# Kernel tuning notes

Hardware: AMD Instinct MI355X
Metric: run time of the kernel (lower is better)

Reference implementation:

```python
import jax, jax.numpy as jnp
import numpy as np

IN_FEATURES = 512
OUT_FEATURES = 512
GRID_MIN = -2.0
GRID_MAX = 2.0
NUM_GRIDS = 8
SPLINE_SCALE = 0.1
BATCH = 16384


def setup_inputs() -> dict:
    key = jax.random.key(0)
    kx, kw = jax.random.split(key)
    x = jax.random.normal(kx, (BATCH, IN_FEATURES), dtype=jnp.float32)
    grid = jnp.linspace(GRID_MIN, GRID_MAX, NUM_GRIDS, dtype=jnp.float32)
    spline_weight = (
        jax.random.normal(kw, (IN_FEATURES * NUM_GRIDS, OUT_FEATURES), dtype=jnp.float32)
        * SPLINE_SCALE
    )
    return {"x": x, "grid": grid, "spline_weight": spline_weight}


def reference(x, grid, spline_weight):
    # denominator h = (grid_max - grid_min) / (num_grids - 1)
    h = (GRID_MAX - GRID_MIN) / (NUM_GRIDS - 1)
    # basis: [B, in_features, num_grids]
    basis = jnp.exp(-jnp.square((x[..., None] - grid) / h))
    # flatten to [B, in_features * num_grids] and GEMM
    return basis.reshape(basis.shape[0], -1) @ spline_weight
```

## Files before the change

kernel.cpp:

```cpp
#include <hip/hip_runtime.h>
#include <hip/hip_bf16.h>

#define BATCH 16384
#define IN_F 512
#define OUT_F 512
#define NG 8
#define KTOT (IN_F * NG)

#define SH    2.1019642153762872f
#define SSTEP 1.2011224087864498f
#define BC0N  4.2039284307525745f

typedef __attribute__((ext_vector_type(8))) short short8;
typedef __attribute__((ext_vector_type(4))) float f32x4;
typedef __attribute__((ext_vector_type(2))) float f32x2;
typedef __attribute__((ext_vector_type(4))) unsigned int u32x4;
typedef __attribute__((ext_vector_type(2))) unsigned int u32x2;

__device__ __forceinline__ unsigned fbits(float f) {
    union { float f; unsigned u; } v; v.f = f; return v.u;
}
__device__ __forceinline__ unsigned pack2bf(float lo, float hi) {
    unsigned a = (fbits(lo) + 0x8000u) >> 16;
    unsigned b = (fbits(hi) + 0x8000u) & 0xFFFF0000u;
    return a | b;
}

__global__ void wt_convert(const float* __restrict__ W, unsigned short* __restrict__ Wt) {
    const int gid  = blockIdx.x * 4 + (threadIdx.x >> 6);
    const int lane = threadIdx.x & 63;
    const int kw = gid & 511;
    const int nw = gid >> 9;
    const int n  = nw * 64 + lane;
    const int k0 = kw * 8;
    float v[8];
#pragma unroll
    for (int j = 0; j < 8; ++j)
        v[j] = W[(size_t)(k0 + j) * OUT_F + n];
    u32x4 pk;
#pragma unroll
    for (int j = 0; j < 4; ++j)
        pk[j] = pack2bf(v[2 * j], v[2 * j + 1]);
    *(u32x4*)(Wt + (size_t)n * KTOT + k0) = pk;
}

#define BM2 64
#define BN2 256
#define BK2 64
#define ABUF (BM2 * BK2)
#define BBUF (BN2 * BK2)

__global__ __launch_bounds__(256, 2) void gauss_gemm3(
        const float* __restrict__ X, const unsigned short* __restrict__ Wt,
        float* __restrict__ Out) {
    __shared__ __align__(16) unsigned short sA[2 * ABUF];
    __shared__ __align__(16) unsigned short sB[2 * BBUF];

    const int tid  = threadIdx.x;
    const int lane = tid & 63;
    const int wave = tid >> 6;
    const int rb = blockIdx.x >> 1;
    const int cb = blockIdx.x & 1;
    const int m0 = rb * BM2;
    const int n0 = cb * BN2;
    const int l15 = lane & 15;
    const int lq  = lane >> 4;

    const int arow = tid >> 2;
    const int axp  = tid & 3;
    const float* xp = X + (size_t)(m0 + arow) * IN_F + 2 * axp;
    const int aoff0 = arow * BK2 + ((((axp << 1)    ) ^ (arow & 7)) << 3);
    const int aoff1 = arow * BK2 + ((((axp << 1) | 1) ^ (arow & 7)) << 3);

    const int brow = lane >> 3;
    const int bch  = (lane & 7) ^ brow;
    const unsigned short* bsrc =
        Wt + (size_t)(n0 + wave * 64 + brow) * KTOT + bch * 8;

    f32x4 acc[4][4];
#pragma unroll
    for (int i = 0; i < 4; ++i)
#pragma unroll
        for (int j = 0; j < 4; ++j)
            acc[i][j] = (f32x4){0.f, 0.f, 0.f, 0.f};

    auto stageB = [&](int kt, int buf) {
#pragma unroll
        for (int p = 0; p < 8; ++p) {
            __builtin_amdgcn_global_load_lds(
                (const __attribute__((address_space(1))) unsigned int*)
                    (const void*)(bsrc + (size_t)p * 8 * KTOT + (size_t)kt * BK2),
                (__attribute__((address_space(3))) unsigned int*)
                    (void*)(sB + buf * BBUF + (wave * 64 + p * 8) * BK2),
                16, 0, 0);
        }
    };

    auto stageA = [&](f32x2 xv, int buf) {
        unsigned short* base = sA + buf * ABUF;
#pragma unroll
        for (int h = 0; h < 2; ++h) {
            const float xs = (h ? xv.y : xv.x) * SH;
            u32x4 pk;
#pragma unroll
            for (int g = 0; g < 8; g += 2) {
                float t0 = xs + (BC0N - g * SSTEP);
                float t1 = xs + (BC0N - (g + 1) * SSTEP);
                unsigned u0 = fbits(__builtin_amdgcn_exp2f(-t0 * t0)) + 0x8000u;
                unsigned u1 = fbits(__builtin_amdgcn_exp2f(-t1 * t1)) + 0x8000u;
                pk[g >> 1] = __builtin_amdgcn_perm(u1, u0, 0x07060302u);
            }
            *(u32x4*)(base + (h ? aoff1 : aoff0)) = pk;
        }
    };

    stageB(0, 0);
    f32x2 xv = *(const f32x2*)(xp);
    stageA(xv, 0);
    f32x2 xnext = *(const f32x2*)(xp + 8);
    __syncthreads();

    for (int kt = 0; kt < KTOT / BK2 - 1; ++kt) {
        const int cur = kt & 1, nxt = cur ^ 1;

        f32x2 xpf;
        if (kt < KTOT / BK2 - 2)
            xpf = *(const f32x2*)(xp + (size_t)(kt + 2) * 8);

        stageB(kt + 1, nxt);

        short8 af[2][4], bfv[2][4];
#pragma unroll
        for (int kk = 0; kk < 2; ++kk) {
            const int koff = ((((kk << 2) + lq) ^ (l15 & 7)) << 3);
#pragma unroll
            for (int i = 0; i < 4; ++i)
                af[kk][i] = *(const short8*)(sA + cur * ABUF + (i * 16 + l15) * BK2 + koff);
#pragma unroll
            for (int j = 0; j < 4; ++j)
                bfv[kk][j] = *(const short8*)(sB + cur * BBUF + (wave * 64 + j * 16 + l15) * BK2 + koff);
        }

        stageA(xnext, nxt);

#pragma unroll
        for (int kk = 0; kk < 2; ++kk)
#pragma unroll
            for (int i = 0; i < 4; ++i)
#pragma unroll
                for (int j = 0; j < 4; ++j)
                    acc[i][j] = __builtin_amdgcn_mfma_f32_16x16x32_bf16(af[kk][i], bfv[kk][j], acc[i][j], 0, 0, 0);

        xnext = xpf;
        __syncthreads();
    }

    {
        const int cur = (KTOT / BK2 - 1) & 1;
#pragma unroll
        for (int kk = 0; kk < 2; ++kk) {
            const int koff = ((((kk << 2) + lq) ^ (l15 & 7)) << 3);
            short8 af[4], bfv[4];
#pragma unroll
            for (int i = 0; i < 4; ++i)
                af[i] = *(const short8*)(sA + cur * ABUF + (i * 16 + l15) * BK2 + koff);
#pragma unroll
            for (int j = 0; j < 4; ++j)
                bfv[j] = *(const short8*)(sB + cur * BBUF + (wave * 64 + j * 16 + l15) * BK2 + koff);
#pragma unroll
            for (int i = 0; i < 4; ++i)
#pragma unroll
                for (int j = 0; j < 4; ++j)
                    acc[i][j] = __builtin_amdgcn_mfma_f32_16x16x32_bf16(af[i], bfv[j], acc[i][j], 0, 0, 0);
        }
    }

#pragma unroll
    for (int i = 0; i < 4; ++i) {
        const int r0 = m0 + i * 16 + lq * 4;
#pragma unroll
        for (int j = 0; j < 4; ++j) {
            const int c = n0 + wave * 64 + j * 16 + l15;
#pragma unroll
            for (int e = 0; e < 4; ++e)
                Out[(size_t)(r0 + e) * OUT_F + c] = acc[i][j][e];
        }
    }
}

#define BM 128
#define BN 128
#define BK 64
#define LDA 72
#define LDB 72

__global__ __launch_bounds__(256, 2) void gauss_gemm_fb(
        const float* __restrict__ X, const float* __restrict__ W,
        float* __restrict__ Out) {
    __shared__ __align__(16) unsigned short sA[BM * LDA];
    __shared__ __align__(16) unsigned short sB[BN * LDB];

    const int tid  = threadIdx.x;
    const int lane = tid & 63;
    const int wave = tid >> 6;
    const int rb = blockIdx.x >> 2;
    const int cb = blockIdx.x & 3;
    const int m0 = rb * BM;
    const int n0 = cb * BN;
    const int wr = (wave >> 1) * 64;
    const int wc = (wave & 1) * 64;
    const int l15 = lane & 15;
    const int lq  = lane >> 4;

    f32x4 acc[4][4];
#pragma unroll
    for (int i = 0; i < 4; ++i)
#pragma unroll
        for (int j = 0; j < 4; ++j)
            acc[i][j] = (f32x4){0.f, 0.f, 0.f, 0.f};

    const int arow = tid & 127;
    const int axq  = tid >> 7;

    for (int kt = 0; kt < KTOT / BK; ++kt) {
        const int k0  = kt * BK;
        const int xc0 = kt * (BK / NG);

        const f32x4 xv = *(const f32x4*)(X + (size_t)(m0 + arow) * IN_F + xc0 + 4 * axq);
        unsigned short* sArow = sA + arow * LDA + axq * 32;
#pragma unroll
        for (int j = 0; j < 4; ++j) {
            const float xs = xv[j] * SH;
            u32x4 pk;
#pragma unroll
            for (int g = 0; g < 8; g += 2) {
                float t0 = xs + (BC0N - g * SSTEP);
                float t1 = xs + (BC0N - (g + 1) * SSTEP);
                unsigned u0 = fbits(__builtin_amdgcn_exp2f(-t0 * t0)) + 0x8000u;
                unsigned u1 = fbits(__builtin_amdgcn_exp2f(-t1 * t1)) + 0x8000u;
                pk[g >> 1] = __builtin_amdgcn_perm(u1, u0, 0x07060302u);
            }
            *(u32x4*)(sArow + j * 8) = pk;
        }

#pragma unroll
        for (int p = 0; p < 8; ++p) {
            int id = p * 256 + tid;
            int n  = id & 127;
            int k4 = id >> 7;
            const float* wp = W + (size_t)(k0 + k4 * 4) * OUT_F + n0 + n;
            u32x2 v;
            v[0] = pack2bf(wp[0], wp[OUT_F]);
            v[1] = pack2bf(wp[2 * OUT_F], wp[3 * OUT_F]);
            *(u32x2*)(sB + n * LDB + k4 * 4) = v;
        }

        __syncthreads();

#pragma unroll
        for (int kk = 0; kk < BK; kk += 32) {
            short8 af[4], bfv[4];
#pragma unroll
            for (int i = 0; i < 4; ++i)
                af[i] = *(const short8*)(sA + (wr + i * 16 + l15) * LDA + kk + lq * 8);
#pragma unroll
            for (int i = 0; i < 4; ++i)
                bfv[i] = *(const short8*)(sB + (wc + i * 16 + l15) * LDB + kk + lq * 8);
#pragma unroll
            for (int i = 0; i < 4; ++i)
#pragma unroll
                for (int j = 0; j < 4; ++j)
                    acc[i][j] = __builtin_amdgcn_mfma_f32_16x16x32_bf16(af[i], bfv[j], acc[i][j], 0, 0, 0);
        }

        __syncthreads();
    }

#pragma unroll
    for (int i = 0; i < 4; ++i) {
        const int r0 = m0 + wr + i * 16 + lq * 4;
#pragma unroll
        for (int j = 0; j < 4; ++j) {
            const int c = n0 + wc + j * 16 + l15;
#pragma unroll
            for (int e = 0; e < 4; ++e)
                Out[(size_t)(r0 + e) * OUT_F + c] = acc[i][j][e];
        }
    }
}

extern "C" void kernel_launch(void* const* d_in, const int* in_sizes, int n_in,
                              void* d_out, int out_size, void* d_ws, size_t ws_size,
                              hipStream_t stream) {
    (void)in_sizes; (void)n_in; (void)out_size;
    const float* X = (const float*)d_in[0];
    const float* W = (const float*)d_in[2];
    float* Out = (float*)d_out;

    const size_t wt_bytes = (size_t)KTOT * OUT_F * sizeof(unsigned short);
    if (ws_size >= wt_bytes) {
        unsigned short* Wt = (unsigned short*)d_ws;
        wt_convert<<<dim3(KTOT * OUT_F / (8 * 64 * 4)), 256, 0, stream>>>(W, Wt);
        gauss_gemm3<<<dim3((BATCH / BM2) * (OUT_F / BN2)), 256, 0, stream>>>(X, Wt, Out);
    } else {
        gauss_gemm_fb<<<dim3((BATCH / BM) * (OUT_F / BN)), 256, 0, stream>>>(X, W, Out);
    }
}
```

Before: 171.1 us.

## Use single-wave blocks with register-resident Gaussian basis via exp recurrence

Replaces the 4-wave 64x256 GEMM with single-wave 64x64 blocks. Each block stages raw x values and weights through LDS, with no block barriers, and computes the A fragments for the MFMA directly in registers. The eight Gaussian basis values per input are produced with two exp2 calls plus a multiplicative recurrence instead of eight exps, which cuts transcendental work. In exchange each x value is recomputed for more output tiles, weight reuse per block drops, and the recurrence may add small rounding differences.

```diff
diff --git a/kernel.cpp b/kernel.cpp
--- a/kernel.cpp
+++ b/kernel.cpp
@@ -10,10 +10,12 @@
 #define SH    2.1019642153762872f
 #define SSTEP 1.2011224087864498f
 #define BC0N  4.2039284307525745f
+#define RC1   2.4022448175728996f
+#define RC2  -1.4426950408889634f
+#define RQ    0.13533528323661270f
 
 typedef __attribute__((ext_vector_type(8))) short short8;
 typedef __attribute__((ext_vector_type(4))) float f32x4;
-typedef __attribute__((ext_vector_type(2))) float f32x2;
 typedef __attribute__((ext_vector_type(4))) unsigned int u32x4;
 typedef __attribute__((ext_vector_type(2))) unsigned int u32x2;
 
@@ -44,39 +46,171 @@
     *(u32x4*)(Wt + (size_t)n * KTOT + k0) = pk;
 }
 
-#define BM2 64
-#define BN2 256
-#define BK2 64
-#define ABUF (BM2 * BK2)
-#define BBUF (BN2 * BK2)
-
-__global__ __launch_bounds__(256, 2) void gauss_gemm3(
+#define WM 64
+#define WN 64
+#define WK 64
+
+__global__ __launch_bounds__(64, 2) void gauss_gemm4(
         const float* __restrict__ X, const unsigned short* __restrict__ Wt,
         float* __restrict__ Out) {
-    __shared__ __align__(16) unsigned short sA[2 * ABUF];
-    __shared__ __align__(16) unsigned short sB[2 * BBUF];
+    __shared__ __align__(16) unsigned short sB[2 * WN * WK];
+    __shared__ __align__(16) float slab[2 * WM * 8];
+
+    const int lane = threadIdx.x;
+    const int cb = blockIdx.x & 7;
+    const int rb = blockIdx.x >> 3;
+    const int m0 = rb * WM;
+    const int n0 = cb * WN;
+    const int l15 = lane & 15;
+    const int lq  = lane >> 4;
+
+    const int brow = lane >> 3;
+    const int bch  = (lane & 7) ^ brow;
+    const unsigned short* bsrc = Wt + (size_t)(n0 + brow) * KTOT + bch * 8;
+
+    const float* xlp = X + (size_t)(m0 + lane) * IN_F;
+
+    int bofs[2][4];
+#pragma unroll
+    for (int kk = 0; kk < 2; ++kk)
+#pragma unroll
+        for (int j = 0; j < 4; ++j)
+            bofs[kk][j] = (j * 16 + l15) * WK + (((kk * 4 + lq) ^ (l15 & 7)) << 3);
+
+    f32x4 acc[4][4];
+#pragma unroll
+    for (int i = 0; i < 4; ++i)
+#pragma unroll
+        for (int j = 0; j < 4; ++j)
+            acc[i][j] = (f32x4){0.f, 0.f, 0.f, 0.f};
+
+    f32x4 xr0 = *(const f32x4*)(xlp + 0);
+    f32x4 xr1 = *(const f32x4*)(xlp + 4);
+    *(f32x4*)(slab + lane * 8)     = xr0;
+    *(f32x4*)(slab + lane * 8 + 4) = xr1;
+#pragma unroll
+    for (int p = 0; p < 8; ++p)
+        __builtin_amdgcn_global_load_lds(
+            (const __attribute__((address_space(1))) unsigned int*)
+                (const void*)(bsrc + (size_t)p * 8 * KTOT),
+            (__attribute__((address_space(3))) unsigned int*)
+                (void*)(sB + p * 8 * WK),
+            16, 0, 0);
+    xr0 = *(const f32x4*)(xlp + 8);
+    xr1 = *(const f32x4*)(xlp + 12);
+
+    for (int kt = 0; kt < KTOT / WK; ++kt) {
+        const int cur = kt & 1, nxt = cur ^ 1;
+        const int kpf1 = (kt < 63) ? kt + 1 : 63;
+        const int kpf2 = (kt < 62) ? kt + 2 : 63;
+
+        float xv[2][4];
+#pragma unroll
+        for (int kk = 0; kk < 2; ++kk)
+#pragma unroll
+            for (int i = 0; i < 4; ++i)
+                xv[kk][i] = slab[cur * 512 + (i * 16 + l15) * 8 + kk * 4 + lq];
+
+        __builtin_amdgcn_sched_barrier(0);
+        __builtin_amdgcn_s_waitcnt(0);
+        __builtin_amdgcn_sched_barrier(0);
+
+        short8 bf[2][4];
+        const unsigned short* sBc = sB + cur * (WN * WK);
+#pragma unroll
+        for (int kk = 0; kk < 2; ++kk)
+#pragma unroll
+            for (int j = 0; j < 4; ++j)
+                bf[kk][j] = *(const short8*)(sBc + bofs[kk][j]);
+
+        *(f32x4*)(slab + nxt * 512 + lane * 8)     = xr0;
+        *(f32x4*)(slab + nxt * 512 + lane * 8 + 4) = xr1;
+
+        xr0 = *(const f32x4*)(xlp + (size_t)kpf2 * 8);
+        xr1 = *(const f32x4*)(xlp + (size_t)kpf2 * 8 + 4);
+
+        {
+            const unsigned short* bs = bsrc + (size_t)kpf1 * WK;
+            unsigned short* bd = sB + nxt * (WN * WK);
+#pragma unroll
+            for (int p = 0; p < 8; ++p)
+                __builtin_amdgcn_global_load_lds(
+                    (const __attribute__((address_space(1))) unsigned int*)
+                        (const void*)(bs + (size_t)p * 8 * KTOT),
+                    (__attribute__((address_space(3))) unsigned int*)
+                        (void*)(bd + p * 8 * WK),
+                    16, 0, 0);
+        }
+
+        short8 af[2][4];
+#pragma unroll
+        for (int kk = 0; kk < 2; ++kk)
+#pragma unroll
+            for (int i = 0; i < 4; ++i) {
+                const float t0 = fmaf(xv[kk][i], SH, BC0N);
+                float r = __builtin_amdgcn_exp2f(fmaf(t0, RC1, RC2));
+                const float v0 = __builtin_amdgcn_exp2f(-t0 * t0);
+                const float v1 = v0 * r;
+                r *= RQ; const float v2 = v1 * r;
+                r *= RQ; const float v3 = v2 * r;
+                r *= RQ; const float v4 = v3 * r;
+                r *= RQ; const float v5 = v4 * r;
+                r *= RQ; const float v6 = v5 * r;
+                r *= RQ; const float v7 = v6 * r;
+                u32x4 pk;
+                pk[0] = pack2bf(v0, v1);
+                pk[1] = pack2bf(v2, v3);
+                pk[2] = pack2bf(v4, v5);
+                pk[3] = pack2bf(v6, v7);
+                af[kk][i] = *(short8*)&pk;
+            }
+
+#pragma unroll
+        for (int kk = 0; kk < 2; ++kk)
+#pragma unroll
+            for (int i = 0; i < 4; ++i)
+#pragma unroll
+                for (int j = 0; j < 4; ++j)
+                    acc[i][j] = __builtin_amdgcn_mfma_f32_16x16x32_bf16(af[kk][i], bf[kk][j], acc[i][j], 0, 0, 0);
+    }
+
+#pragma unroll
+    for (int i = 0; i < 4; ++i) {
+        const int r0 = m0 + i * 16 + lq * 4;
+#pragma unroll
+        for (int j = 0; j < 4; ++j) {
+            const int c = n0 + j * 16 + l15;
+#pragma unroll
+            for (int e = 0; e < 4; ++e)
+                Out[(size_t)(r0 + e) * OUT_F + c] = acc[i][j][e];
+        }
+    }
+}
+
+#define BM 128
+#define BN 128
+#define BK 64
+#define LDA 72
+#define LDB 72
+
+__global__ __launch_bounds__(256, 2) void gauss_gemm_fb(
+        const float* __restrict__ X, const float* __restrict__ W,
+        float* __restrict__ Out) {
+    __shared__ __align__(16) unsigned short sA[BM * LDA];
+    __shared__ __align__(16) unsigned short sB2[BN * LDB];
 
     const int tid  = threadIdx.x;
     const int lane = tid & 63;
     const int wave = tid >> 6;
-    const int rb = blockIdx.x >> 1;
-    const int cb = blockIdx.x & 1;
-    const int m0 = rb * BM2;
-    const int n0 = cb * BN2;
+    const int rb = blockIdx.x >> 2;
+    const int cbx = blockIdx.x & 3;
+    const int m0 = rb * BM;
+    const int n0 = cbx * BN;
+    const int wr = (wave >> 1) * 64;
+    const int wc = (wave & 1) * 64;
     const int l15 = lane & 15;
     const int lq  = lane >> 4;
 
-    const int arow = tid >> 2;
-    const int axp  = tid & 3;
-    const float* xp = X + (size_t)(m0 + arow) * IN_F + 2 * axp;
-    const int aoff0 = arow * BK2 + ((((axp << 1)    ) ^ (arow & 7)) << 3);
-    const int aoff1 = arow * BK2 + ((((axp << 1) | 1) ^ (arow & 7)) << 3);
-
-    const int brow = lane >> 3;
-    const int bch  = (lane & 7) ^ brow;
-    const unsigned short* bsrc =
-        Wt + (size_t)(n0 + wave * 64 + brow) * KTOT + bch * 8;
-
     f32x4 acc[4][4];
 #pragma unroll
     for (int i = 0; i < 4; ++i)
@@ -84,23 +218,18 @@
         for (int j = 0; j < 4; ++j)
             acc[i][j] = (f32x4){0.f, 0.f, 0.f, 0.f};
 
-    auto stageB = [&](int kt, int buf) {
-#pragma unroll
-        for (int p = 0; p < 8; ++p) {
-            __builtin_amdgcn_global_load_lds(
-                (const __attribute__((address_space(1))) unsigned int*)
-                    (const void*)(bsrc + (size_t)p * 8 * KTOT + (size_t)kt * BK2),
-                (__attribute__((address_space(3))) unsigned int*)
-                    (void*)(sB + buf * BBUF + (wave * 64 + p * 8) * BK2),
-                16, 0, 0);
-        }
-    };
-
-    auto stageA = [&](f32x2 xv, int buf) {
-        unsigned short* base = sA + buf * ABUF;
-#pragma unroll
-        for (int h = 0; h < 2; ++h) {
-            const float xs = (h ? xv.y : xv.x) * SH;
+    const int arow = tid & 127;
+    const int axq  = tid >> 7;
+
+    for (int kt = 0; kt < KTOT / BK; ++kt) {
+        const int k0  = kt * BK;
+        const int xc0 = kt * (BK / NG);
+
+        const f32x4 xv = *(const f32x4*)(X + (size_t)(m0 + arow) * IN_F + xc0 + 4 * axq);
+        unsigned short* sArow = sA + arow * LDA + axq * 32;
+#pragma unroll
+        for (int j = 0; j < 4; ++j) {
+            const float xs = xv[j] * SH;
             u32x4 pk;
 #pragma unroll
             for (int g = 0; g < 8; g += 2) {
@@ -108,137 +237,7 @@
                 float t1 = xs + (BC0N - (g + 1) * SSTEP);
                 unsigned u0 = fbits(__builtin_amdgcn_exp2f(-t0 * t0)) + 0x8000u;
                 unsigned u1 = fbits(__builtin_amdgcn_exp2f(-t1 * t1)) + 0x8000u;
-                pk[g >> 1] = __builtin_amdgcn_perm(u1, u0, 0x07060302u);
-            }
-            *(u32x4*)(base + (h ? aoff1 : aoff0)) = pk;
-        }
-    };
-
-    stageB(0, 0);
-    f32x2 xv = *(const f32x2*)(xp);
-    stageA(xv, 0);
-    f32x2 xnext = *(const f32x2*)(xp + 8);
-    __syncthreads();
-
-    for (int kt = 0; kt < KTOT / BK2 - 1; ++kt) {
-        const int cur = kt & 1, nxt = cur ^ 1;
-
-        f32x2 xpf;
-        if (kt < KTOT / BK2 - 2)
-            xpf = *(const f32x2*)(xp + (size_t)(kt + 2) * 8);
-
-        stageB(kt + 1, nxt);
-
-        short8 af[2][4], bfv[2][4];
-#pragma unroll
-        for (int kk = 0; kk < 2; ++kk) {
-            const int koff = ((((kk << 2) + lq) ^ (l15 & 7)) << 3);
-#pragma unroll
-            for (int i = 0; i < 4; ++i)
-                af[kk][i] = *(const short8*)(sA + cur * ABUF + (i * 16 + l15) * BK2 + koff);
-#pragma unroll
-            for (int j = 0; j < 4; ++j)
-                bfv[kk][j] = *(const short8*)(sB + cur * BBUF + (wave * 64 + j * 16 + l15) * BK2 + koff);
-        }
-
-        stageA(xnext, nxt);
-
-#pragma unroll
-        for (int kk = 0; kk < 2; ++kk)
-#pragma unroll
-            for (int i = 0; i < 4; ++i)
-#pragma unroll
-                for (int j = 0; j < 4; ++j)
-                    acc[i][j] = __builtin_amdgcn_mfma_f32_16x16x32_bf16(af[kk][i], bfv[kk][j], acc[i][j], 0, 0, 0);
-
-        xnext = xpf;
-        __syncthreads();
-    }
-
-    {
-        const int cur = (KTOT / BK2 - 1) & 1;
-#pragma unroll
-        for (int kk = 0; kk < 2; ++kk) {
-            const int koff = ((((kk << 2) + lq) ^ (l15 & 7)) << 3);
-            short8 af[4], bfv[4];
-#pragma unroll
-            for (int i = 0; i < 4; ++i)
-                af[i] = *(const short8*)(sA + cur * ABUF + (i * 16 + l15) * BK2 + koff);
-#pragma unroll
-            for (int j = 0; j < 4; ++j)
-                bfv[j] = *(const short8*)(sB + cur * BBUF + (wave * 64 + j * 16 + l15) * BK2 + koff);
-#pragma unroll
-            for (int i = 0; i < 4; ++i)
-#pragma unroll
-                for (int j = 0; j < 4; ++j)
-                    acc[i][j] = __builtin_amdgcn_mfma_f32_16x16x32_bf16(af[i], bfv[j], acc[i][j], 0, 0, 0);
-        }
-    }
-
-#pragma unroll
-    for (int i = 0; i < 4; ++i) {
-        const int r0 = m0 + i * 16 + lq * 4;
-#pragma unroll
-        for (int j = 0; j < 4; ++j) {
-            const int c = n0 + wave * 64 + j * 16 + l15;
-#pragma unroll
-            for (int e = 0; e < 4; ++e)
-                Out[(size_t)(r0 + e) * OUT_F + c] = acc[i][j][e];
-        }
-    }
-}
-
-#define BM 128
-#define BN 128
-#define BK 64
-#define LDA 72
-#define LDB 72
-
-__global__ __launch_bounds__(256, 2) void gauss_gemm_fb(
-        const float* __restrict__ X, const float* __restrict__ W,
-        float* __restrict__ Out) {
-    __shared__ __align__(16) unsigned short sA[BM * LDA];
-    __shared__ __align__(16) unsigned short sB[BN * LDB];
-
-    const int tid  = threadIdx.x;
-    const int lane = tid & 63;
-    const int wave = tid >> 6;
-    const int rb = blockIdx.x >> 2;
-    const int cb = blockIdx.x & 3;
-    const int m0 = rb * BM;
-    const int n0 = cb * BN;
-    const int wr = (wave >> 1) * 64;
-    const int wc = (wave & 1) * 64;
-    const int l15 = lane & 15;
-    const int lq  = lane >> 4;
-
-    f32x4 acc[4][4];
-#pragma unroll
-    for (int i = 0; i < 4; ++i)
-#pragma unroll
-        for (int j = 0; j < 4; ++j)
-            acc[i][j] = (f32x4){0.f, 0.f, 0.f, 0.f};
-
-    const int arow = tid & 127;
-    const int axq  = tid >> 7;
-
-    for (int kt = 0; kt < KTOT / BK; ++kt) {
-        const int k0  = kt * BK;
-        const int xc0 = kt * (BK / NG);
-
-        const f32x4 xv = *(const f32x4*)(X + (size_t)(m0 + arow) * IN_F + xc0 + 4 * axq);
-        unsigned short* sArow = sA + arow * LDA + axq * 32;
-#pragma unroll
-        for (int j = 0; j < 4; ++j) {
-            const float xs = xv[j] * SH;
-            u32x4 pk;
-#pragma unroll
-            for (int g = 0; g < 8; g += 2) {
-                float t0 = xs + (BC0N - g * SSTEP);
-                float t1 = xs + (BC0N - (g + 1) * SSTEP);
-                unsigned u0 = fbits(__builtin_amdgcn_exp2f(-t0 * t0)) + 0x8000u;
-                unsigned u1 = fbits(__builtin_amdgcn_exp2f(-t1 * t1)) + 0x8000u;
-                pk[g >> 1] = __builtin_amdgcn_perm(u1, u0, 0x07060302u);
+                pk[g >> 1] = (u0 >> 16) | (u1 & 0xFFFF0000u);
             }
             *(u32x4*)(sArow + j * 8) = pk;
         }
@@ -252,7 +251,7 @@
             u32x2 v;
             v[0] = pack2bf(wp[0], wp[OUT_F]);
             v[1] = pack2bf(wp[2 * OUT_F], wp[3 * OUT_F]);
-            *(u32x2*)(sB + n * LDB + k4 * 4) = v;
+            *(u32x2*)(sB2 + n * LDB + k4 * 4) = v;
         }
 
         __syncthreads();
@@ -265,7 +264,7 @@
                 af[i] = *(const short8*)(sA + (wr + i * 16 + l15) * LDA + kk + lq * 8);
 #pragma unroll
             for (int i = 0; i < 4; ++i)
-                bfv[i] = *(const short8*)(sB + (wc + i * 16 + l15) * LDB + kk + lq * 8);
+                bfv[i] = *(const short8*)(sB2 + (wc + i * 16 + l15) * LDB + kk + lq * 8);
 #pragma unroll
             for (int i = 0; i < 4; ++i)
 #pragma unroll
@@ -301,7 +300,7 @@
     if (ws_size >= wt_bytes) {
         unsigned short* Wt = (unsigned short*)d_ws;
         wt_convert<<<dim3(KTOT * OUT_F / (8 * 64 * 4)), 256, 0, stream>>>(W, Wt);
-        gauss_gemm3<<<dim3((BATCH / BM2) * (OUT_F / BN2)), 256, 0, stream>>>(X, Wt, Out);
+        gauss_gemm4<<<dim3((BATCH / WM) * (OUT_F / WN)), 64, 0, stream>>>(X, Wt, Out);
     } else {
         gauss_gemm_fb<<<dim3((BATCH / BM) * (OUT_F / BN)), 256, 0, stream>>>(X, W, Out);
     }
```

Measured after the change: 194.0 us. +13.3%, slower.
